# Performance work log

Hardware: AMD Instinct MI355X
Metric: run time of the kernel (lower is better)

The kernel has to match this reference:

```python
import jax, jax.numpy as jnp
import numpy as np

B, T, N, H = 256, 128, 128, 256  # batch, window, n_input_series, encoder hidden


def setup_inputs() -> dict:
    key = jax.random.key(0)
    ks = jax.random.split(key, 11)
    s = 0.05
    return {
        "input_data": jax.random.normal(ks[0], (B, T, N), jnp.float32),
        # attn_layer_hidden: Linear(2H -> T)
        "W_ah": jax.random.normal(ks[1], (T, 2 * H), jnp.float32) * s,
        "b_ah": jax.random.normal(ks[2], (T,), jnp.float32) * s,
        # attn_layer_input: Linear(T -> 1)
        "W_ai": jax.random.normal(ks[3], (1, T), jnp.float32) * s,
        "b_ai": jax.random.normal(ks[4], (1,), jnp.float32) * s,
        # attn_layer: Linear(T -> 1)
        "W_a": jax.random.normal(ks[5], (1, T), jnp.float32) * s,
        "b_a": jax.random.normal(ks[6], (1,), jnp.float32) * s,
        # LSTM(N -> H), gate order i,f,g,o (PyTorch)
        "W_ih": jax.random.normal(ks[7], (4 * H, N), jnp.float32) * s,
        "W_hh": jax.random.normal(ks[8], (4 * H, H), jnp.float32) * s,
        "b_ih": jax.random.normal(ks[9], (4 * H,), jnp.float32) * s,
        "b_hh": jax.random.normal(ks[10], (4 * H,), jnp.float32) * s,
    }


def reference(input_data, W_ah, b_ah, W_ai, b_ai, W_a, b_a, W_ih, W_hh, b_ih, b_hh):
    b, t_len, n = input_data.shape
    h_dim = W_hh.shape[1]
    dt = input_data.dtype

    # attn_layer_input part is time-invariant: [B, N] (one scalar per series)
    ipart = jnp.einsum('btn,t->bn', input_data, W_ai[0]) + b_ai[0]

    xs = jnp.swapaxes(input_data, 0, 1)  # [T, B, N]

    def step(carry, x_t):
        h, c = carry  # each [B, H]
        hc = jnp.concatenate([h, c], axis=-1)          # [B, 2H]
        hpart = hc @ W_ah.T + b_ah                      # [B, T]
        z = jnp.tanh(hpart[:, None, :] + ipart[:, :, None])  # [B, N, T]
        score = jnp.einsum('bnt,t->bn', z, W_a[0]) + b_a[0]   # [B, N]
        attn = jax.nn.softmax(score, axis=-1)
        wx = attn * x_t                                 # weighted input [B, N]
        gates = wx @ W_ih.T + b_ih + h @ W_hh.T + b_hh  # [B, 4H]
        i, f, g, o = jnp.split(gates, 4, axis=-1)
        i = jax.nn.sigmoid(i)
        f = jax.nn.sigmoid(f)
        g = jnp.tanh(g)
        o = jax.nn.sigmoid(o)
        c2 = f * c + i * g
        h2 = o * jnp.tanh(c2)
        return (h2, c2), (wx, h2)

    h0 = jnp.zeros((b, h_dim), dt)
    c0 = jnp.zeros((b, h_dim), dt)
    (_, _), (iw, ie) = jax.lax.scan(step, (h0, c0), xs)
    input_weighted = jnp.swapaxes(iw, 0, 1)  # [B, T, N]
    input_encoded = jnp.swapaxes(ie, 0, 1)   # [B, T, H]
    return input_weighted, input_encoded
```

## Files before the change

### kernel.cpp

```cpp
#include <hip/hip_runtime.h>
#include <cstdint>

#define NB 256
#define NT 128
#define NS 128
#define NH 256

#define NTHR 1024
#define NWG  256
#define NGRP 64
#define GBAT 4
#define UPW  64

#define HC_OFF  0
#define CNT_OFF 131072

typedef _Float16 f16;
typedef _Float16 f16x2 __attribute__((ext_vector_type(2)));
typedef _Float16 f16x8 __attribute__((ext_vector_type(8)));
typedef float    f32x4 __attribute__((ext_vector_type(4)));

#define SAH 528
#define SAG 392

__device__ __forceinline__ f16x2 pk(float a, float b) {
  f16x2 r; r.x = (f16)a; r.y = (f16)b; return r;
}
__device__ __forceinline__ f16x8 pack8(const float* s) {
  float4 v0 = *(const float4*)s, v1 = *(const float4*)(s + 4);
  f16x8 r;
  r[0] = (f16)v0.x; r[1] = (f16)v0.y; r[2] = (f16)v0.z; r[3] = (f16)v0.w;
  r[4] = (f16)v1.x; r[5] = (f16)v1.y; r[6] = (f16)v1.z; r[7] = (f16)v1.w;
  return r;
}
__device__ __forceinline__ void awr(uint32_t* p, uint32_t v) {
  __hip_atomic_store(p, v, __ATOMIC_RELAXED, __HIP_MEMORY_SCOPE_AGENT);
}
__device__ __forceinline__ uint32_t ard(uint32_t* p) {
  return __hip_atomic_load(p, __ATOMIC_RELAXED, __HIP_MEMORY_SCOPE_AGENT);
}
__device__ __forceinline__ void cinc(uint32_t* p) {
  __hip_atomic_fetch_add(p, 1u, __ATOMIC_RELAXED, __HIP_MEMORY_SCOPE_AGENT);
}
__device__ __forceinline__ void cwait(uint32_t* p, uint32_t tgt) {
  while (ard(p) < tgt) __builtin_amdgcn_s_sleep(1);
}

struct __align__(16) Sm {
  f16   wahp[128 * SAH];
  f16   hcp[5 * SAH];
  f16   agxp[5 * SAG];
  float PW[128 * 5 * 2];
  union {
    float pacc[8][2][16][4];
    float sp[2][4][128];
  } u;
  float gacc[256 * 4];
  float gbias[256];
  float cbuf[256];
  float w2a[128];
  float bah[128];
};

__global__ void enc_init(uint32_t* ws) {
  int i = blockIdx.x * blockDim.x + threadIdx.x;
  if (i < 65536) ws[HC_OFF + i] = 0u;
  if (i < 1024)  ws[CNT_OFF + i] = 0u;
}

__global__ __launch_bounds__(NTHR, 4) void enc_main(
    const float* __restrict__ x,    const float* __restrict__ W_ah,
    const float* __restrict__ b_ah, const float* __restrict__ W_ai,
    const float* __restrict__ b_ai, const float* __restrict__ W_a,
    const float* __restrict__ b_a,  const float* __restrict__ W_ih,
    const float* __restrict__ W_hh, const float* __restrict__ b_ih,
    const float* __restrict__ b_hh, float* __restrict__ out_iw,
    float* __restrict__ out_ie,     uint32_t* __restrict__ ws)
{
  __shared__ Sm sm;
  const int tid  = threadIdx.x;
  const int wg   = blockIdx.x;
  const int xcd  = wg & 7, slot = wg >> 3;
  const int g    = xcd * 8 + (slot >> 2);
  const int gid  = slot & 3;
  const int b0   = g * GBAT;
  const int u0   = gid * UPW;

  const int wv = tid >> 6, ln = tid & 63;
  const int bn = ln & 15, kq = ln >> 4;

  uint32_t* cnt = ws + CNT_OFF + g * 16;

  f16x8 wfrag[12];
  {
    const int lr = wv * 16 + bn;
    const int grow = (lr >> 6) * 256 + u0 + (lr & 63);
    #pragma unroll
    for (int kk = 0; kk < 4; ++kk)
      wfrag[kk] = pack8(W_ih + (size_t)grow * NS + kk * 32 + kq * 8);
    #pragma unroll
    for (int kk = 4; kk < 12; ++kk)
      wfrag[kk] = pack8(W_hh + (size_t)grow * NH + (kk - 4) * 32 + kq * 8);
  }

  #pragma unroll
  for (int i = 0; i < 8; ++i) {
    int idx = i * NTHR + tid;
    int r = idx >> 6, c = idx & 63;
    f16x8 v = pack8(W_ah + (size_t)r * 512 + c * 8);
    *(f16x8*)&sm.wahp[(size_t)r * SAH + c * 8] = v;
  }
  if (tid < 256) {
    int grow = (tid >> 6) * 256 + u0 + (tid & 63);
    sm.gbias[tid] = b_ih[grow] + b_hh[grow];
    sm.cbuf[tid] = 0.f;
  }
  if (tid < 128) { sm.w2a[tid] = 2.f * W_a[tid]; sm.bah[tid] = b_ah[tid]; }
  if (tid < 512) sm.hcp[4 * SAH + tid] = (f16)0.f;
  if (tid < 384) sm.agxp[4 * SAG + tid] = (f16)0.f;

  const int n_s = tid & 127, bq_s = (tid >> 7) & 3, ts_s = tid >> 9;
  float ev;
  {
    const float* xb = x + (size_t)(b0 + bq_s) * NT * NS;
    float a = 0.f;
    #pragma unroll 4
    for (int t = 0; t < NT; ++t) a = fmaf(xb[(size_t)t * NS + n_s], W_ai[t], a);
    ev = __expf(2.f * (a + b_ai[0]));
  }
  float S0;
  { float s = b_a[0]; for (int i = 0; i < 128; ++i) s += W_a[i]; S0 = s; }

  __syncthreads();

  for (int t = 0; t < NT; ++t) {
    const int par = t & 1;
    float xv0 = 0.f, xv1 = 0.f;
    if (wv < 4) {
      const float* xr = x + ((size_t)(b0 + wv) * NT + t) * NS;
      xv0 = xr[ln]; xv1 = xr[ln + 64];
    }
    if (t > 0) {
      if (tid == 0) cwait(cnt, 4u * (uint32_t)t);
      __syncthreads();
    }
    {
      uint32_t* hcb = ws + HC_OFF + ((size_t)par * NGRP + g) * 1024;
      uint32_t v = ard(hcb + tid);
      f16x2 pv = __builtin_bit_cast(f16x2, v);
      int b = tid >> 8, u = tid & 255;
      sm.hcp[b * SAH + u] = pv.x;
      sm.hcp[b * SAH + 256 + u] = pv.y;
      sm.agxp[b * SAG + 128 + u] = pv.x;
    }
    __syncthreads();
    {
      const int tile = wv & 7, half = wv >> 3;
      f32x4 acc = {0.f, 0.f, 0.f, 0.f};
      const int br = (bn < 4) ? bn : 4;
      #pragma unroll
      for (int j = 0; j < 8; ++j) {
        int kk = half * 8 + j;
        f16x8 a = *(const f16x8*)&sm.wahp[(size_t)(tile * 16 + bn) * SAH + kk * 32 + kq * 8];
        f16x8 b = *(const f16x8*)&sm.hcp[(size_t)br * SAH + kk * 32 + kq * 8];
        acc = __builtin_amdgcn_mfma_f32_16x16x32_f16(a, b, acc, 0, 0, 0);
      }
      if (bn < 4) {
        #pragma unroll
        for (int r = 0; r < 4; ++r)
          sm.u.pacc[tile][half][kq * 4 + r][bn] = acc[r];
      }
    }
    __syncthreads();
    if (tid < 512) {
      int tl = tid >> 2, b = tid & 3;
      float p = sm.u.pacc[tl >> 4][0][tl & 15][b] + sm.u.pacc[tl >> 4][1][tl & 15][b];
      float pe = __expf(2.f * (p + sm.bah[tl]));
      sm.PW[(tl * 5 + b) * 2]     = pe;
      sm.PW[(tl * 5 + b) * 2 + 1] = sm.w2a[tl];
    }
    __syncthreads();
    {
      float s = 0.f;
      #pragma unroll 8
      for (int i = 0; i < 64; ++i) {
        int tp = ts_s * 64 + i;
        float2 pw = *(const float2*)&sm.PW[(tp * 5 + bq_s) * 2];
        float pe = fmaf(pw.x, ev, 1.f);
        s = fmaf(pw.y, __builtin_amdgcn_rcpf(pe), s);
      }
      sm.u.sp[ts_s][bq_s][n_s] = s;
    }
    __syncthreads();
    if (wv < 4) {
      float sA = S0 - (sm.u.sp[0][wv][ln] + sm.u.sp[1][wv][ln]);
      float sB = S0 - (sm.u.sp[0][wv][ln + 64] + sm.u.sp[1][wv][ln + 64]);
      float m = fmaxf(sA, sB);
      #pragma unroll
      for (int o = 32; o; o >>= 1) m = fmaxf(m, __shfl_xor(m, o));
      float eA = __expf(sA - m), eB = __expf(sB - m);
      float ss = eA + eB;
      #pragma unroll
      for (int o = 32; o; o >>= 1) ss += __shfl_xor(ss, o);
      float rs = 1.f / ss;
      float wxA = eA * rs * xv0, wxB = eB * rs * xv1;
      sm.agxp[wv * SAG + ln] = (f16)wxA;
      sm.agxp[wv * SAG + ln + 64] = (f16)wxB;
      if (wv == gid) {
        float* ow = out_iw + ((size_t)(b0 + wv) * NT + t) * NS;
        ow[ln] = wxA; ow[ln + 64] = wxB;
      }
    }
    __syncthreads();
    {
      const int br = (bn < 4) ? bn : 4;
      f32x4 acc = {0.f, 0.f, 0.f, 0.f};
      #pragma unroll
      for (int kk = 0; kk < 12; ++kk) {
        f16x8 a = *(const f16x8*)&sm.agxp[(size_t)br * SAG + kk * 32 + kq * 8];
        acc = __builtin_amdgcn_mfma_f32_16x16x32_f16(a, wfrag[kk], acc, 0, 0, 0);
      }
      if (ln < 16)
        *(f32x4*)&sm.gacc[(wv * 16 + ln) * 4] = acc;
    }
    __syncthreads();
    if (tid < 256) {
      const int b = tid >> 6, ul = tid & 63;
      float gi = sm.gacc[(ul) * 4 + b]       + sm.gbias[ul];
      float gf = sm.gacc[(64 + ul) * 4 + b]  + sm.gbias[64 + ul];
      float gg = sm.gacc[(128 + ul) * 4 + b] + sm.gbias[128 + ul];
      float go = sm.gacc[(192 + ul) * 4 + b] + sm.gbias[192 + ul];
      float ii = 1.f / (1.f + __expf(-gi));
      float ff = 1.f / (1.f + __expf(-gf));
      float gt = 1.f - 2.f / (1.f + __expf(2.f * gg));
      float oo = 1.f / (1.f + __expf(-go));
      float c2 = ff * sm.cbuf[ul * 4 + b] + ii * gt;
      float h2 = oo * (1.f - 2.f / (1.f + __expf(2.f * c2)));
      sm.cbuf[ul * 4 + b] = c2;
      out_ie[((size_t)(b0 + b) * NT + t) * NH + u0 + ul] = h2;
      uint32_t* dst = ws + HC_OFF + ((size_t)(1 - par) * NGRP + g) * 1024 +
                      b * 256 + u0 + ul;
      awr(dst, __builtin_bit_cast(uint32_t, pk(h2, c2)));
    }
    __syncthreads();
    if (tid == 0) cinc(cnt);
  }
}

extern "C" void kernel_launch(void* const* d_in, const int* in_sizes, int n_in,
                              void* d_out, int out_size, void* d_ws, size_t ws_size,
                              hipStream_t stream) {
  const float* x    = (const float*)d_in[0];
  const float* W_ah = (const float*)d_in[1];
  const float* b_ah = (const float*)d_in[2];
  const float* W_ai = (const float*)d_in[3];
  const float* b_ai = (const float*)d_in[4];
  const float* W_a  = (const float*)d_in[5];
  const float* b_a  = (const float*)d_in[6];
  const float* W_ih = (const float*)d_in[7];
  const float* W_hh = (const float*)d_in[8];
  const float* b_ih = (const float*)d_in[9];
  const float* b_hh = (const float*)d_in[10];
  float* out_iw = (float*)d_out;
  float* out_ie = (float*)d_out + (size_t)NB * NT * NS;
  uint32_t* ws = (uint32_t*)d_ws;

  hipLaunchKernelGGL(enc_init, dim3(256), dim3(256), 0, stream, ws);
  hipLaunchKernelGGL(enc_main, dim3(NWG), dim3(NTHR), 0, stream,
                     x, W_ah, b_ah, W_ai, b_ai, W_a, b_a, W_ih, W_hh, b_ih, b_hh,
                     out_iw, out_ie, ws);
}
```

Measured before the change: 732.8 us.

## Ping-pong two independent batch sub-groups per workgroup to hide recurrence sync

Each workgroup now serves two independent 2-batch recurrence groups instead of one 4-batch group, each with its own counter and h/c exchange buffers. The phases are interleaved: group 1's cross-workgroup wait and h/c load, and its attention-hidden MFMA, are placed alongside group 0's attention and gate work. The intent is to overlap the global-memory spin-wait latency of one group with compute for the other. The attention score loop is also reworked to combine two terms under one reciprocal. In exchange, each step has roughly twice as many block barriers, and the MFMA tiles use only 2 of 16 rows, so more MFMA work is wasted.

Result: slower. 1.228 ms (+67.6%).

```diff
diff --git a/kernel.cpp b/kernel.cpp
--- a/kernel.cpp
+++ b/kernel.cpp
@@ -5,12 +5,8 @@
 #define NT 128
 #define NS 128
 #define NH 256
-
 #define NTHR 1024
 #define NWG  256
-#define NGRP 64
-#define GBAT 4
-#define UPW  64
 
 #define HC_OFF  0
 #define CNT_OFF 131072
@@ -20,8 +16,9 @@
 typedef _Float16 f16x8 __attribute__((ext_vector_type(8)));
 typedef float    f32x4 __attribute__((ext_vector_type(4)));
 
-#define SAH 528
-#define SAG 392
+#define SW 528
+#define SH 528
+#define SA 136
 
 __device__ __forceinline__ f16x2 pk(float a, float b) {
   f16x2 r; r.x = (f16)a; r.y = (f16)b; return r;
@@ -47,25 +44,21 @@
 }
 
 struct __align__(16) Sm {
-  f16   wahp[128 * SAH];
-  f16   hcp[5 * SAH];
-  f16   agxp[5 * SAG];
-  float PW[128 * 5 * 2];
-  union {
-    float pacc[8][2][16][4];
-    float sp[2][4][128];
-  } u;
-  float gacc[256 * 4];
+  f16   wahp[128 * SW];
+  f16   hcp[2][3 * SH];
+  f16   act[3 * SA];
+  float PW[2 * 128 * 2];
+  float sp[4][2][128];
+  float gacc[256][2];
   float gbias[256];
-  float cbuf[256];
-  float w2a[128];
+  float cbuf[2][64][2];
   float bah[128];
 };
 
 __global__ void enc_init(uint32_t* ws) {
   int i = blockIdx.x * blockDim.x + threadIdx.x;
   if (i < 65536) ws[HC_OFF + i] = 0u;
-  if (i < 1024)  ws[CNT_OFF + i] = 0u;
+  if (i < 2048)  ws[CNT_OFF + i] = 0u;
 }
 
 __global__ __launch_bounds__(NTHR, 4) void enc_main(
@@ -81,15 +74,18 @@
   const int tid  = threadIdx.x;
   const int wg   = blockIdx.x;
   const int xcd  = wg & 7, slot = wg >> 3;
-  const int g    = xcd * 8 + (slot >> 2);
+  const int pair = xcd * 8 + (slot >> 2);
   const int gid  = slot & 3;
-  const int b0   = g * GBAT;
-  const int u0   = gid * UPW;
+  const int g0   = pair * 2, g1 = pair * 2 + 1;
+  const int bb0  = g0 * 2,  bb1 = g1 * 2;
+  const int u0   = gid * 64;
 
   const int wv = tid >> 6, ln = tid & 63;
   const int bn = ln & 15, kq = ln >> 4;
-
-  uint32_t* cnt = ws + CNT_OFF + g * 16;
+  const int br2 = (bn < 2) ? bn : 2;
+
+  uint32_t* cnt0 = ws + CNT_OFF + (size_t)g0 * 16;
+  uint32_t* cnt1 = ws + CNT_OFF + (size_t)g1 * 16;
 
   f16x8 wfrag[12];
   {
@@ -108,25 +104,32 @@
     int idx = i * NTHR + tid;
     int r = idx >> 6, c = idx & 63;
     f16x8 v = pack8(W_ah + (size_t)r * 512 + c * 8);
-    *(f16x8*)&sm.wahp[(size_t)r * SAH + c * 8] = v;
+    *(f16x8*)&sm.wahp[(size_t)r * SW + c * 8] = v;
   }
   if (tid < 256) {
     int grow = (tid >> 6) * 256 + u0 + (tid & 63);
     sm.gbias[tid] = b_ih[grow] + b_hh[grow];
-    sm.cbuf[tid] = 0.f;
-  }
-  if (tid < 128) { sm.w2a[tid] = 2.f * W_a[tid]; sm.bah[tid] = b_ah[tid]; }
-  if (tid < 512) sm.hcp[4 * SAH + tid] = (f16)0.f;
-  if (tid < 384) sm.agxp[4 * SAG + tid] = (f16)0.f;
-
-  const int n_s = tid & 127, bq_s = (tid >> 7) & 3, ts_s = tid >> 9;
-  float ev;
+    int b = tid >> 7, tp = tid & 127;
+    sm.PW[(b * 128 + tp) * 2 + 1] = 2.f * W_a[tp];
+  }
+  if (tid < 128) sm.bah[tid] = b_ah[tid];
+  if (tid < 256) { sm.cbuf[tid >> 7][(tid >> 1) & 63][tid & 1] = 0.f; }
+  if (tid < 512) { sm.hcp[0][2 * SH + tid] = (f16)0.f; sm.hcp[1][2 * SH + tid] = (f16)0.f; }
+  if (tid < 128) sm.act[2 * SA + tid] = (f16)0.f;
+
+  const int n_s = tid & 127, b_s = (tid >> 7) & 1, ts_s = tid >> 8;
+  float ev0, ev1;
   {
-    const float* xb = x + (size_t)(b0 + bq_s) * NT * NS;
+    const float* xb = x + (size_t)(bb0 + b_s) * NT * NS;
     float a = 0.f;
     #pragma unroll 4
     for (int t = 0; t < NT; ++t) a = fmaf(xb[(size_t)t * NS + n_s], W_ai[t], a);
-    ev = __expf(2.f * (a + b_ai[0]));
+    ev0 = __expf(2.f * (a + b_ai[0]));
+    const float* xc = x + (size_t)(bb1 + b_s) * NT * NS;
+    float a2 = 0.f;
+    #pragma unroll 4
+    for (int t = 0; t < NT; ++t) a2 = fmaf(xc[(size_t)t * NS + n_s], W_ai[t], a2);
+    ev1 = __expf(2.f * (a2 + b_ai[0]));
   }
   float S0;
   { float s = b_a[0]; for (int i = 0; i < 128; ++i) s += W_a[i]; S0 = s; }
@@ -134,67 +137,69 @@
   __syncthreads();
 
   for (int t = 0; t < NT; ++t) {
-    const int par = t & 1;
+    const int par = t & 1, par2 = 1 - par;
     float xv0 = 0.f, xv1 = 0.f;
     if (wv < 4) {
-      const float* xr = x + ((size_t)(b0 + wv) * NT + t) * NS;
+      const int bb = (wv >> 1) ? bb1 : bb0;
+      const float* xr = x + ((size_t)(bb + (wv & 1)) * NT + t) * NS;
       xv0 = xr[ln]; xv1 = xr[ln + 64];
     }
     if (t > 0) {
-      if (tid == 0) cwait(cnt, 4u * (uint32_t)t);
+      if (tid == 0) cwait(cnt0, 4u * (uint32_t)t);
       __syncthreads();
     }
-    {
-      uint32_t* hcb = ws + HC_OFF + ((size_t)par * NGRP + g) * 1024;
-      uint32_t v = ard(hcb + tid);
+    if (tid < 512) {
+      uint32_t v = ard(ws + HC_OFF + (((size_t)par * 128 + g0) * 2 + (tid >> 8)) * 256 + (tid & 255));
       f16x2 pv = __builtin_bit_cast(f16x2, v);
       int b = tid >> 8, u = tid & 255;
-      sm.hcp[b * SAH + u] = pv.x;
-      sm.hcp[b * SAH + 256 + u] = pv.y;
-      sm.agxp[b * SAG + 128 + u] = pv.x;
-    }
-    __syncthreads();
-    {
-      const int tile = wv & 7, half = wv >> 3;
+      sm.hcp[0][b * SH + u] = pv.x;
+      sm.hcp[0][b * SH + 256 + u] = pv.y;
+    }
+    __syncthreads();
+    if (wv < 8) {
       f32x4 acc = {0.f, 0.f, 0.f, 0.f};
-      const int br = (bn < 4) ? bn : 4;
+      #pragma unroll
+      for (int kk = 0; kk < 16; ++kk) {
+        f16x8 a = *(const f16x8*)&sm.wahp[(size_t)(wv * 16 + bn) * SW + kk * 32 + kq * 8];
+        f16x8 b = *(const f16x8*)&sm.hcp[0][(size_t)br2 * SH + kk * 32 + kq * 8];
+        acc = __builtin_amdgcn_mfma_f32_16x16x32_f16(a, b, acc, 0, 0, 0);
+      }
+      if (bn < 2) {
+        #pragma unroll
+        for (int r = 0; r < 4; ++r) {
+          int tp = wv * 16 + kq * 4 + r;
+          sm.PW[(bn * 128 + tp) * 2] = __expf(2.f * (acc[r] + sm.bah[tp]));
+        }
+      }
+    } else if (wv == 8) {
+      if (ln == 0 && t > 0) cwait(cnt1, 4u * (uint32_t)t);
       #pragma unroll
       for (int j = 0; j < 8; ++j) {
-        int kk = half * 8 + j;
-        f16x8 a = *(const f16x8*)&sm.wahp[(size_t)(tile * 16 + bn) * SAH + kk * 32 + kq * 8];
-        f16x8 b = *(const f16x8*)&sm.hcp[(size_t)br * SAH + kk * 32 + kq * 8];
-        acc = __builtin_amdgcn_mfma_f32_16x16x32_f16(a, b, acc, 0, 0, 0);
-      }
-      if (bn < 4) {
-        #pragma unroll
-        for (int r = 0; r < 4; ++r)
-          sm.u.pacc[tile][half][kq * 4 + r][bn] = acc[r];
-      }
-    }
-    __syncthreads();
-    if (tid < 512) {
-      int tl = tid >> 2, b = tid & 3;
-      float p = sm.u.pacc[tl >> 4][0][tl & 15][b] + sm.u.pacc[tl >> 4][1][tl & 15][b];
-      float pe = __expf(2.f * (p + sm.bah[tl]));
-      sm.PW[(tl * 5 + b) * 2]     = pe;
-      sm.PW[(tl * 5 + b) * 2 + 1] = sm.w2a[tl];
+        int w = j * 64 + ln;
+        uint32_t v = ard(ws + HC_OFF + (((size_t)par * 128 + g1) * 2 + (w >> 8)) * 256 + (w & 255));
+        f16x2 pv = __builtin_bit_cast(f16x2, v);
+        int b = w >> 8, u = w & 255;
+        sm.hcp[1][b * SH + u] = pv.x;
+        sm.hcp[1][b * SH + 256 + u] = pv.y;
+      }
     }
     __syncthreads();
     {
       float s = 0.f;
       #pragma unroll 8
-      for (int i = 0; i < 64; ++i) {
-        int tp = ts_s * 64 + i;
-        float2 pw = *(const float2*)&sm.PW[(tp * 5 + bq_s) * 2];
-        float pe = fmaf(pw.x, ev, 1.f);
-        s = fmaf(pw.y, __builtin_amdgcn_rcpf(pe), s);
-      }
-      sm.u.sp[ts_s][bq_s][n_s] = s;
-    }
-    __syncthreads();
-    if (wv < 4) {
-      float sA = S0 - (sm.u.sp[0][wv][ln] + sm.u.sp[1][wv][ln]);
-      float sB = S0 - (sm.u.sp[0][wv][ln + 64] + sm.u.sp[1][wv][ln + 64]);
+      for (int i = 0; i < 16; ++i) {
+        float4 rd = *(const float4*)&sm.PW[(b_s * 128 + ts_s * 32 + 2 * i) * 2];
+        float d1 = fmaf(rd.x, ev0, 1.f);
+        float d2 = fmaf(rd.z, ev0, 1.f);
+        float num = fmaf(rd.w, d1, rd.y * d2);
+        s = fmaf(num, __builtin_amdgcn_rcpf(d1 * d2), s);
+      }
+      sm.sp[ts_s][b_s][n_s] = s;
+    }
+    __syncthreads();
+    if (wv < 2) {
+      float sA = S0 - (sm.sp[0][wv][ln] + sm.sp[1][wv][ln] + sm.sp[2][wv][ln] + sm.sp[3][wv][ln]);
+      float sB = S0 - (sm.sp[0][wv][ln + 64] + sm.sp[1][wv][ln + 64] + sm.sp[2][wv][ln + 64] + sm.sp[3][wv][ln + 64]);
       float m = fmaxf(sA, sB);
       #pragma unroll
       for (int o = 32; o; o >>= 1) m = fmaxf(m, __shfl_xor(m, o));
@@ -204,46 +209,131 @@
       for (int o = 32; o; o >>= 1) ss += __shfl_xor(ss, o);
       float rs = 1.f / ss;
       float wxA = eA * rs * xv0, wxB = eB * rs * xv1;
-      sm.agxp[wv * SAG + ln] = (f16)wxA;
-      sm.agxp[wv * SAG + ln + 64] = (f16)wxB;
-      if (wv == gid) {
-        float* ow = out_iw + ((size_t)(b0 + wv) * NT + t) * NS;
+      sm.act[wv * SA + ln] = (f16)wxA;
+      sm.act[wv * SA + ln + 64] = (f16)wxB;
+      if (gid == wv) {
+        float* ow = out_iw + ((size_t)(bb0 + wv) * NT + t) * NS;
         ow[ln] = wxA; ow[ln + 64] = wxB;
       }
     }
     __syncthreads();
     {
-      const int br = (bn < 4) ? bn : 4;
       f32x4 acc = {0.f, 0.f, 0.f, 0.f};
       #pragma unroll
-      for (int kk = 0; kk < 12; ++kk) {
-        f16x8 a = *(const f16x8*)&sm.agxp[(size_t)br * SAG + kk * 32 + kq * 8];
+      for (int kk = 0; kk < 4; ++kk) {
+        f16x8 a = *(const f16x8*)&sm.act[(size_t)br2 * SA + kk * 32 + kq * 8];
         acc = __builtin_amdgcn_mfma_f32_16x16x32_f16(a, wfrag[kk], acc, 0, 0, 0);
       }
-      if (ln < 16)
-        *(f32x4*)&sm.gacc[(wv * 16 + ln) * 4] = acc;
-    }
-    __syncthreads();
-    if (tid < 256) {
-      const int b = tid >> 6, ul = tid & 63;
-      float gi = sm.gacc[(ul) * 4 + b]       + sm.gbias[ul];
-      float gf = sm.gacc[(64 + ul) * 4 + b]  + sm.gbias[64 + ul];
-      float gg = sm.gacc[(128 + ul) * 4 + b] + sm.gbias[128 + ul];
-      float go = sm.gacc[(192 + ul) * 4 + b] + sm.gbias[192 + ul];
+      #pragma unroll
+      for (int kk = 4; kk < 12; ++kk) {
+        f16x8 a = *(const f16x8*)&sm.hcp[0][(size_t)br2 * SH + (kk - 4) * 32 + kq * 8];
+        acc = __builtin_amdgcn_mfma_f32_16x16x32_f16(a, wfrag[kk], acc, 0, 0, 0);
+      }
+      if (ln < 16) { sm.gacc[wv * 16 + ln][0] = acc[0]; sm.gacc[wv * 16 + ln][1] = acc[1]; }
+    }
+    __syncthreads();
+    if (wv < 8) {
+      f32x4 acc = {0.f, 0.f, 0.f, 0.f};
+      #pragma unroll
+      for (int kk = 0; kk < 16; ++kk) {
+        f16x8 a = *(const f16x8*)&sm.wahp[(size_t)(wv * 16 + bn) * SW + kk * 32 + kq * 8];
+        f16x8 b = *(const f16x8*)&sm.hcp[1][(size_t)br2 * SH + kk * 32 + kq * 8];
+        acc = __builtin_amdgcn_mfma_f32_16x16x32_f16(a, b, acc, 0, 0, 0);
+      }
+      if (bn < 2) {
+        #pragma unroll
+        for (int r = 0; r < 4; ++r) {
+          int tp = wv * 16 + kq * 4 + r;
+          sm.PW[(bn * 128 + tp) * 2] = __expf(2.f * (acc[r] + sm.bah[tp]));
+        }
+      }
+    } else if (tid < 640) {
+      const int l = tid - 512, b = l >> 6, ul = l & 63;
+      float gi = sm.gacc[ul][b]        + sm.gbias[ul];
+      float gf = sm.gacc[64 + ul][b]   + sm.gbias[64 + ul];
+      float gg = sm.gacc[128 + ul][b]  + sm.gbias[128 + ul];
+      float go = sm.gacc[192 + ul][b]  + sm.gbias[192 + ul];
       float ii = 1.f / (1.f + __expf(-gi));
       float ff = 1.f / (1.f + __expf(-gf));
       float gt = 1.f - 2.f / (1.f + __expf(2.f * gg));
       float oo = 1.f / (1.f + __expf(-go));
-      float c2 = ff * sm.cbuf[ul * 4 + b] + ii * gt;
+      float c2 = ff * sm.cbuf[0][ul][b] + ii * gt;
       float h2 = oo * (1.f - 2.f / (1.f + __expf(2.f * c2)));
-      sm.cbuf[ul * 4 + b] = c2;
-      out_ie[((size_t)(b0 + b) * NT + t) * NH + u0 + ul] = h2;
-      uint32_t* dst = ws + HC_OFF + ((size_t)(1 - par) * NGRP + g) * 1024 +
-                      b * 256 + u0 + ul;
-      awr(dst, __builtin_bit_cast(uint32_t, pk(h2, c2)));
-    }
-    __syncthreads();
-    if (tid == 0) cinc(cnt);
+      sm.cbuf[0][ul][b] = c2;
+      out_ie[((size_t)(bb0 + b) * NT + t) * NH + u0 + ul] = h2;
+      awr(ws + HC_OFF + (((size_t)par2 * 128 + g0) * 2 + b) * 256 + u0 + ul,
+          __builtin_bit_cast(uint32_t, pk(h2, c2)));
+    }
+    __syncthreads();
+    if (tid == 0) cinc(cnt0);
+    {
+      float s = 0.f;
+      #pragma unroll 8
+      for (int i = 0; i < 16; ++i) {
+        float4 rd = *(const float4*)&sm.PW[(b_s * 128 + ts_s * 32 + 2 * i) * 2];
+        float d1 = fmaf(rd.x, ev1, 1.f);
+        float d2 = fmaf(rd.z, ev1, 1.f);
+        float num = fmaf(rd.w, d1, rd.y * d2);
+        s = fmaf(num, __builtin_amdgcn_rcpf(d1 * d2), s);
+      }
+      sm.sp[ts_s][b_s][n_s] = s;
+    }
+    __syncthreads();
+    if (wv == 2 || wv == 3) {
+      const int b = wv - 2;
+      float sA = S0 - (sm.sp[0][b][ln] + sm.sp[1][b][ln] + sm.sp[2][b][ln] + sm.sp[3][b][ln]);
+      float sB = S0 - (sm.sp[0][b][ln + 64] + sm.sp[1][b][ln + 64] + sm.sp[2][b][ln + 64] + sm.sp[3][b][ln + 64]);
+      float m = fmaxf(sA, sB);
+      #pragma unroll
+      for (int o = 32; o; o >>= 1) m = fmaxf(m, __shfl_xor(m, o));
+      float eA = __expf(sA - m), eB = __expf(sB - m);
+      float ss = eA + eB;
+      #pragma unroll
+      for (int o = 32; o; o >>= 1) ss += __shfl_xor(ss, o);
+      float rs = 1.f / ss;
+      float wxA = eA * rs * xv0, wxB = eB * rs * xv1;
+      sm.act[b * SA + ln] = (f16)wxA;
+      sm.act[b * SA + ln + 64] = (f16)wxB;
+      if (gid == 2 + b) {
+        float* ow = out_iw + ((size_t)(bb1 + b) * NT + t) * NS;
+        ow[ln] = wxA; ow[ln + 64] = wxB;
+      }
+    }
+    __syncthreads();
+    {
+      f32x4 acc = {0.f, 0.f, 0.f, 0.f};
+      #pragma unroll
+      for (int kk = 0; kk < 4; ++kk) {
+        f16x8 a = *(const f16x8*)&sm.act[(size_t)br2 * SA + kk * 32 + kq * 8];
+        acc = __builtin_amdgcn_mfma_f32_16x16x32_f16(a, wfrag[kk], acc, 0, 0, 0);
+      }
+      #pragma unroll
+      for (int kk = 4; kk < 12; ++kk) {
+        f16x8 a = *(const f16x8*)&sm.hcp[1][(size_t)br2 * SH + (kk - 4) * 32 + kq * 8];
+        acc = __builtin_amdgcn_mfma_f32_16x16x32_f16(a, wfrag[kk], acc, 0, 0, 0);
+      }
+      if (ln < 16) { sm.gacc[wv * 16 + ln][0] = acc[0]; sm.gacc[wv * 16 + ln][1] = acc[1]; }
+    }
+    __syncthreads();
+    if (tid < 128) {
+      const int b = tid >> 6, ul = tid & 63;
+      float gi = sm.gacc[ul][b]        + sm.gbias[ul];
+      float gf = sm.gacc[64 + ul][b]   + sm.gbias[64 + ul];
+      float gg = sm.gacc[128 + ul][b]  + sm.gbias[128 + ul];
+      float go = sm.gacc[192 + ul][b]  + sm.gbias[192 + ul];
+      float ii = 1.f / (1.f + __expf(-gi));
+      float ff = 1.f / (1.f + __expf(-gf));
+      float gt = 1.f - 2.f / (1.f + __expf(2.f * gg));
+      float oo = 1.f / (1.f + __expf(-go));
+      float c2 = ff * sm.cbuf[1][ul][b] + ii * gt;
+      float h2 = oo * (1.f - 2.f / (1.f + __expf(2.f * c2)));
+      sm.cbuf[1][ul][b] = c2;
+      out_ie[((size_t)(bb1 + b) * NT + t) * NH + u0 + ul] = h2;
+      awr(ws + HC_OFF + (((size_t)par2 * 128 + g1) * 2 + b) * 256 + u0 + ul,
+          __builtin_bit_cast(uint32_t, pk(h2, c2)));
+    }
+    __syncthreads();
+    if (tid == 0) cinc(cnt1);
   }
 }
 
```
